# Performance work log

Measured on AMD Instinct MI355X. Metric: run time of the kernel, lower is better.

## Reference

```python
import jax, jax.numpy as jnp
import numpy as np

B, T, C = 4, 2048, 1024
N_HEAD = 16
HEAD_DIM = C // N_HEAD


def setup_inputs() -> dict:
    key = jax.random.key(0)
    k1, k2, k3 = jax.random.split(key, 3)
    scale = 1.0 / np.sqrt(C)
    return {
        "x": jax.random.normal(k1, (B, T, C), dtype=jnp.float32),
        "W_attn": jax.random.normal(k2, (C, 3 * C), dtype=jnp.float32) * scale,
        "b_attn": jnp.zeros((3 * C,), dtype=jnp.float32),
        "W_proj": jax.random.normal(k3, (C, C), dtype=jnp.float32) * scale,
        "b_proj": jnp.zeros((C,), dtype=jnp.float32),
    }


def reference(x, W_attn, b_attn, W_proj, b_proj):
    Bt, Tt, Ct = x.shape
    qkv = x @ W_attn + b_attn                      # [B,T,3C]
    q, k, v = jnp.split(qkv, 3, axis=-1)
    # [B,T,C] -> [B,H,T,D]
    def heads(t):
        return t.reshape(Bt, Tt, N_HEAD, HEAD_DIM).transpose(0, 2, 1, 3)
    q, k, v = heads(q), heads(k), heads(v)
    att = jnp.einsum("bhqd,bhkd->bhqk", q, k) * (1.0 / np.sqrt(HEAD_DIM))
    causal = jnp.tril(jnp.ones((Tt, Tt), dtype=bool))
    att = jnp.where(causal, att, jnp.finfo(att.dtype).min)
    att = jax.nn.softmax(att, axis=-1)
    # dropout = 0.0 (eval mode): identity
    y = jnp.einsum("bhqk,bhkd->bhqd", att, v)      # [B,H,T,D]
    y = y.transpose(0, 2, 1, 3).reshape(Bt, Tt, Ct)
    return y @ W_proj + b_proj
```

## Files before the change

kernel.cpp:

```cpp
#include <hip/hip_runtime.h>
#include <hip/hip_bf16.h>
#include <cstdint>

#define B_SZ 4
#define T_SZ 2048
#define C_SZ 1024
#define H_SZ 16
#define D_SZ 64
#define BT_SZ (B_SZ * T_SZ)
#define C3_SZ (3 * C_SZ)
#define NKC (C_SZ / 32)

typedef __attribute__((ext_vector_type(8))) short bf16x8;
typedef __attribute__((ext_vector_type(4))) float f32x4;
typedef __attribute__((ext_vector_type(4))) unsigned short ushort4v;
typedef __attribute__((ext_vector_type(4))) unsigned int uint4v;

typedef __attribute__((address_space(3))) unsigned int lds_u32;
typedef __attribute__((address_space(1))) const unsigned int glb_u32;

__device__ __forceinline__ unsigned short f2bf(float f) {
  unsigned u = __builtin_bit_cast(unsigned, f);
  u += 0x7fffu + ((u >> 16) & 1u);
  return (unsigned short)(u >> 16);
}

__device__ __forceinline__ unsigned packbf2(float lo, float hi) {
  return __builtin_amdgcn_perm(__builtin_bit_cast(unsigned, hi),
                               __builtin_bit_cast(unsigned, lo), 0x07060302u);
}

__device__ __forceinline__ void gll16(const unsigned short* g,
                                      unsigned short* l) {
  __builtin_amdgcn_global_load_lds((glb_u32*)g, (lds_u32*)l, 16, 0, 0);
}


__device__ __forceinline__ void pack_x_task(const float* __restrict__ x,
                                            unsigned short* __restrict__ Af,
                                            int task, int lane) {
  const int quad = lane >> 4, n = lane & 15;
  const int tb = task >> 5, kc = task & 31;
  const float* src = x + (size_t)(tb * 16 + n) * C_SZ + kc * 32 + quad * 8;
  float4 a = *(const float4*)src;
  float4 b = *(const float4*)(src + 4);
  ushort4v o0, o1;
  o0[0] = f2bf(a.x); o0[1] = f2bf(a.y); o0[2] = f2bf(a.z); o0[3] = f2bf(a.w);
  o1[0] = f2bf(b.x); o1[1] = f2bf(b.y); o1[2] = f2bf(b.z); o1[3] = f2bf(b.w);
  unsigned short* dst = Af + ((size_t)((tb * NKC + kc) * 4 + quad) * 16 + n) * 8;
  *(ushort4v*)dst = o0;
  *(ushort4v*)(dst + 4) = o1;
}

__device__ __forceinline__ void pack_w_task(const float* __restrict__ W,
                                            unsigned short* __restrict__ Wb,
                                            int N, int task, int lane) {
  const int quad = lane >> 4, n = lane & 15;
  const int nt = task >> 5, kc = task & 31;
  const int col = nt * 16 + n;
  const int k0 = kc * 32 + quad * 8;
  ushort4v o0, o1;
#pragma unroll
  for (int i = 0; i < 4; ++i) o0[i] = f2bf(W[(size_t)(k0 + i) * N + col]);
#pragma unroll
  for (int i = 0; i < 4; ++i) o1[i] = f2bf(W[(size_t)(k0 + 4 + i) * N + col]);
  unsigned short* dst = Wb + ((size_t)((nt * NKC + kc) * 4 + quad) * 16 + n) * 8;
  *(ushort4v*)dst = o0;
  *(ushort4v*)(dst + 4) = o1;
}

__global__ __launch_bounds__(256) void pack_all(
    const float* __restrict__ x, const float* __restrict__ Wa,
    const float* __restrict__ Wp, unsigned short* __restrict__ Af,
    unsigned short* __restrict__ Wab, unsigned short* __restrict__ Wpb) {
  const int bx = blockIdx.x;
  const int sub = threadIdx.x >> 6;
  const int lane = threadIdx.x & 63;
  if (bx < 4096) {
    pack_x_task(x, Af, bx * 4 + sub, lane);
  } else if (bx < 4096 + 1536) {
    pack_w_task(Wa, Wab, C3_SZ, (bx - 4096) * 4 + sub, lane);
  } else {
    pack_w_task(Wp, Wpb, C_SZ, (bx - 5632) * 4 + sub, lane);
  }
}

__device__ __forceinline__ void gemm128_mainloop(
    const unsigned short* __restrict__ A, const unsigned short* __restrict__ B,
    int tbB, int ntB, unsigned short* smem, f32x4 acc[4][4]) {
  const int tid = threadIdx.x;
  const int w = tid >> 6, lane = tid & 63;
  const int quad = lane >> 4, n = lane & 15;
  const int wr = w >> 1, wc = w & 1;
  unsigned short* smemA = smem;
  unsigned short* smemB = smem + 8192;

  for (int kc0 = 0; kc0 < NKC; kc0 += 2) {
#pragma unroll
    for (int i2 = 0; i2 < 2; ++i2) {
      const int i = 2 * w + i2;
      const unsigned short* gA =
          A + ((size_t)(tbB + i) * NKC + kc0) * 512 + lane * 8;
      const unsigned short* gB =
          B + ((size_t)(ntB + i) * NKC + kc0) * 512 + lane * 8;
      gll16(gA, smemA + i * 1024);
      gll16(gA + 512, smemA + i * 1024 + 512);
      gll16(gB, smemB + i * 1024);
      gll16(gB + 512, smemB + i * 1024 + 512);
    }
    __syncthreads();
#pragma unroll
    for (int kcl = 0; kcl < 2; ++kcl) {
      bf16x8 af[4], bfr[4];
#pragma unroll
      for (int m = 0; m < 4; ++m)
        af[m] = *(const bf16x8*)(smemA + (wr * 4 + m) * 1024 +
                                 (kcl * 4 + quad) * 128 + n * 8);
#pragma unroll
      for (int nn = 0; nn < 4; ++nn)
        bfr[nn] = *(const bf16x8*)(smemB + (wc * 4 + nn) * 1024 +
                                   (kcl * 4 + quad) * 128 + n * 8);
#pragma unroll
      for (int m = 0; m < 4; ++m)
#pragma unroll
        for (int nn = 0; nn < 4; ++nn)
          acc[m][nn] = __builtin_amdgcn_mfma_f32_16x16x32_bf16(
              af[m], bfr[nn], acc[m][nn], 0, 0, 0);
    }
    __syncthreads();
  }
}

__global__ __launch_bounds__(256) void qkv_mfma(
    const unsigned short* __restrict__ Af, const unsigned short* __restrict__ Wab,
    const float* __restrict__ bias, unsigned short* __restrict__ Qf,
    unsigned short* __restrict__ Kf, unsigned short* __restrict__ Vf) {
  __shared__ unsigned short smem[16384];
  const int tid = threadIdx.x;
  const int w = tid >> 6, lane = tid & 63;
  const int quad = lane >> 4, n = lane & 15;
  const int wr = w >> 1, wc = w & 1;
  const int bx = blockIdx.x, by = blockIdx.y;
  f32x4 acc[4][4];
#pragma unroll
  for (int m = 0; m < 4; ++m)
#pragma unroll
    for (int nn = 0; nn < 4; ++nn) acc[m][nn] = (f32x4){0.f, 0.f, 0.f, 0.f};

  gemm128_mainloop(Af, Wab, by * 8, bx * 8, smem, acc);

  const int cb = bx * 128 + wc * 64;
  const int which = cb >> 10;
  const int h = (cb & 1023) >> 6;
  const int gr0 = by * 128 + wr * 64;
  const int b = gr0 >> 11;
  const int t0 = gr0 & 2047;
  const size_t bhoff = (size_t)(b * H_SZ + h) * (T_SZ * D_SZ);
  float bfl[4];
#pragma unroll
  for (int nn = 0; nn < 4; ++nn) bfl[nn] = bias[cb + nn * 16 + n];

  if (which < 2) {
    unsigned short* dst = ((which == 0) ? Qf : Kf) + bhoff;
    const float scl = (which == 0) ? 0.18033688f : 1.0f;
#pragma unroll
    for (int m = 0; m < 4; ++m) {
      const int tb = (t0 + m * 16) >> 4;
#pragma unroll
      for (int nn = 0; nn < 4; ++nn) {
        const int dc = nn >> 1;
        const int qd = (nn & 1) * 2 + (n >> 3);
        const int jq = n & 7;
#pragma unroll
        for (int r = 0; r < 4; ++r) {
          const int nq = quad * 4 + r;
          dst[((size_t)((tb * 2 + dc) * 4 + qd)) * 128 + nq * 8 + jq] =
              f2bf((acc[m][nn][r] + bfl[nn]) * scl);
        }
      }
    }
  } else {
    unsigned short* dst = Vf + bhoff;
    const int gb0 = t0 >> 5;
#pragma unroll
    for (int m = 0; m < 4; ++m) {
      const int gb = gb0 + (m >> 1);
#pragma unroll
      for (int nn = 0; nn < 4; ++nn) {
#pragma unroll
        for (int r = 0; r < 4; ++r) {
          dst[((size_t)((gb * 4 + nn) * 4 + quad)) * 128 + n * 8 + (m & 1) * 4 + r] =
              f2bf(acc[m][nn][r] + bfl[nn]);
        }
      }
    }
  }
}

__global__ __launch_bounds__(256) void proj_mfma(
    const unsigned short* __restrict__ Yf, const unsigned short* __restrict__ Wpb,
    const float* __restrict__ bias, float* __restrict__ out) {
  __shared__ unsigned short smem[16384];
  const int tid = threadIdx.x;
  const int w = tid >> 6, lane = tid & 63;
  const int quad = lane >> 4, n = lane & 15;
  const int wr = w >> 1, wc = w & 1;
  const int bx = blockIdx.x, by = blockIdx.y;
  f32x4 acc[4][4];
#pragma unroll
  for (int m = 0; m < 4; ++m)
#pragma unroll
    for (int nn = 0; nn < 4; ++nn) acc[m][nn] = (f32x4){0.f, 0.f, 0.f, 0.f};

  gemm128_mainloop(Yf, Wpb, by * 8, bx * 8, smem, acc);

  const int cb = bx * 128 + wc * 64;
  const int gr0 = by * 128 + wr * 64;
  float bfl[4];
#pragma unroll
  for (int nn = 0; nn < 4; ++nn) bfl[nn] = bias[cb + nn * 16 + n];
#pragma unroll
  for (int m = 0; m < 4; ++m)
#pragma unroll
    for (int nn = 0; nn < 4; ++nn)
#pragma unroll
      for (int r = 0; r < 4; ++r)
        out[(size_t)(gr0 + m * 16 + quad * 4 + r) * C_SZ + cb + nn * 16 + n] =
            acc[m][nn][r] + bfl[nn];
}

__global__ __launch_bounds__(64) void attn_mfma(
    const unsigned short* __restrict__ Qf,
    const unsigned short* __restrict__ Kf,
    const unsigned short* __restrict__ Vf, unsigned short* __restrict__ Yf) {
  const int lane = threadIdx.x;
  const int quad = lane >> 4;
  const int n = lane & 15;
  const int bx = blockIdx.x;
  const int qt = 31 - (bx >> 6);
  const int bh = bx & 63;
  const int b = bh >> 4, h = bh & 15;
  const int wq0 = qt * 64;
  const size_t bhoff = (size_t)bh * (T_SZ * D_SZ);
  const bf16x8* Qp = (const bf16x8*)(Qf + bhoff);
  const bf16x8* Kp = (const bf16x8*)(Kf + bhoff);
  const bf16x8* Vp = (const bf16x8*)(Vf + bhoff);

  bf16x8 qfr[4][2];
#pragma unroll
  for (int m = 0; m < 4; ++m) {
    const int tb = (wq0 >> 4) + m;
#pragma unroll
    for (int dc = 0; dc < 2; ++dc)
      qfr[m][dc] = Qp[((tb * 2 + dc) * 4 + quad) * 16 + n];
  }

  bf16x8 kfr[4][2], vfr[2][4];
  f32x4 O[4][4];
  f32x4 ls[4];
#pragma unroll
  for (int m = 0; m < 4; ++m) {
    ls[m] = (f32x4){0.f, 0.f, 0.f, 0.f};
#pragma unroll
    for (int dv = 0; dv < 4; ++dv) O[m][dv] = (f32x4){0.f, 0.f, 0.f, 0.f};
  }

#pragma unroll
  for (int s = 0; s < 4; ++s) {
    kfr[s][0] = Kp[((s * 2 + 0) * 4 + quad) * 16 + n];
    kfr[s][1] = Kp[((s * 2 + 1) * 4 + quad) * 16 + n];
  }

  for (int kt = 0; kt < qt; ++kt) {
#pragma unroll
    for (int g = 0; g < 2; ++g) {
      const int gb = kt * 2 + g;
#pragma unroll
      for (int dv = 0; dv < 4; ++dv)
        vfr[g][dv] = Vp[((gb * 4 + dv) * 4 + quad) * 16 + n];
    }
#pragma unroll
    for (int m = 0; m < 4; ++m) {
      f32x4 st[4];
#pragma unroll
      for (int s = 0; s < 4; ++s) {
        f32x4 z = {0.f, 0.f, 0.f, 0.f};
        z = __builtin_amdgcn_mfma_f32_16x16x32_bf16(kfr[s][0], qfr[m][0], z, 0, 0, 0);
        z = __builtin_amdgcn_mfma_f32_16x16x32_bf16(kfr[s][1], qfr[m][1], z, 0, 0, 0);
        st[s] = z;
      }
      if (m == 3) {
        const int tb0 = (kt + 1) * 4;
#pragma unroll
        for (int s = 0; s < 4; ++s) {
          kfr[s][0] = Kp[(((tb0 + s) * 2 + 0) * 4 + quad) * 16 + n];
          kfr[s][1] = Kp[(((tb0 + s) * 2 + 1) * 4 + quad) * 16 + n];
        }
      }
      uint4v pw[2];
#pragma unroll
      for (int s = 0; s < 4; ++s) {
        float pr[4];
#pragma unroll
        for (int r = 0; r < 4; ++r) {
          pr[r] = __builtin_amdgcn_exp2f(st[s][r]);
          ls[m][r] += pr[r];
        }
        pw[s >> 1][(s & 1) * 2 + 0] = packbf2(pr[0], pr[1]);
        pw[s >> 1][(s & 1) * 2 + 1] = packbf2(pr[2], pr[3]);
      }
#pragma unroll
      for (int g = 0; g < 2; ++g) {
        const bf16x8 pg = __builtin_bit_cast(bf16x8, pw[g]);
#pragma unroll
        for (int dv = 0; dv < 4; ++dv)
          O[m][dv] = __builtin_amdgcn_mfma_f32_16x16x32_bf16(
              pg, vfr[g][dv], O[m][dv], 0, 0, 0);
      }
    }
  }

  {
#pragma unroll
    for (int g = 0; g < 2; ++g) {
      const int gb = qt * 2 + g;
#pragma unroll
      for (int dv = 0; dv < 4; ++dv)
        vfr[g][dv] = Vp[((gb * 4 + dv) * 4 + quad) * 16 + n];
    }
#pragma unroll
    for (int m = 0; m < 4; ++m) {
      f32x4 st[4];
#pragma unroll
      for (int s = 0; s < 4; ++s) {
        f32x4 z = {0.f, 0.f, 0.f, 0.f};
        if (s <= m) {
          z = __builtin_amdgcn_mfma_f32_16x16x32_bf16(kfr[s][0], qfr[m][0], z, 0, 0, 0);
          z = __builtin_amdgcn_mfma_f32_16x16x32_bf16(kfr[s][1], qfr[m][1], z, 0, 0, 0);
        }
        st[s] = z;
      }
      uint4v pw[2] = {(uint4v){0, 0, 0, 0}, (uint4v){0, 0, 0, 0}};
#pragma unroll
      for (int s = 0; s < 4; ++s) {
        if (s <= m) {
          float pr[4];
#pragma unroll
          for (int r = 0; r < 4; ++r) {
            float v = st[s][r];
            if (s == m && quad * 4 + r > n) v = -1e30f;
            pr[r] = __builtin_amdgcn_exp2f(v);
            ls[m][r] += pr[r];
          }
          pw[s >> 1][(s & 1) * 2 + 0] = packbf2(pr[0], pr[1]);
          pw[s >> 1][(s & 1) * 2 + 1] = packbf2(pr[2], pr[3]);
        }
      }
#pragma unroll
      for (int g = 0; g < 2; ++g) {
        if (g * 2 <= m) {
          const bf16x8 pg = __builtin_bit_cast(bf16x8, pw[g]);
#pragma unroll
          for (int dv = 0; dv < 4; ++dv)
            O[m][dv] = __builtin_amdgcn_mfma_f32_16x16x32_bf16(
                pg, vfr[g][dv], O[m][dv], 0, 0, 0);
        }
      }
    }
  }

#pragma unroll
  for (int m = 0; m < 4; ++m) {
    float lt = ls[m][0] + ls[m][1] + ls[m][2] + ls[m][3];
    lt += __shfl_xor(lt, 16);
    lt += __shfl_xor(lt, 32);
    const float inv = 1.0f / lt;
    float iv[4];
#pragma unroll
    for (int r = 0; r < 4; ++r) iv[r] = __shfl(inv, quad * 4 + r);
    const int tb = (b * T_SZ + wq0 + m * 16) >> 4;
#pragma unroll
    for (int dv = 0; dv < 4; ++dv) {
      const int kc = h * 2 + (dv >> 1);
      const int qa = (dv & 1) * 2 + (n >> 3);
      const int ja = n & 7;
#pragma unroll
      for (int r = 0; r < 4; ++r) {
        const int na = quad * 4 + r;
        Yf[((size_t)((tb * NKC + kc) * 4 + qa)) * 128 + na * 8 + ja] =
            f2bf(O[m][dv][r] * iv[r]);
      }
    }
  }
}

extern "C" void kernel_launch(void* const* d_in, const int* in_sizes, int n_in,
                              void* d_out, int out_size, void* d_ws,
                              size_t ws_size, hipStream_t stream) {
  const float* x = (const float*)d_in[0];
  const float* W_attn = (const float*)d_in[1];
  const float* b_attn = (const float*)d_in[2];
  const float* W_proj = (const float*)d_in[3];
  const float* b_proj = (const float*)d_in[4];
  float* out = (float*)d_out;

  const size_t perbf = (size_t)B_SZ * H_SZ * T_SZ * D_SZ;
  unsigned short* Af = (unsigned short*)d_ws;
  unsigned short* Wab = Af + (size_t)BT_SZ * C_SZ;
  unsigned short* Wpb = Wab + (size_t)C_SZ * C3_SZ;
  unsigned short* Qf = Wpb + (size_t)C_SZ * C_SZ;
  unsigned short* Kf = Qf + perbf;
  unsigned short* Vf = Kf + perbf;
  unsigned short* Yf = Vf + perbf;

  pack_all<<<6144, 256, 0, stream>>>(x, W_attn, W_proj, Af, Wab, Wpb);
  qkv_mfma<<<dim3(C3_SZ / 128, BT_SZ / 128), 256, 0, stream>>>(
      Af, Wab, b_attn, Qf, Kf, Vf);
  attn_mfma<<<dim3(32 * B_SZ * H_SZ), 64, 0, stream>>>(Qf, Kf, Vf, Yf);
  proj_mfma<<<dim3(C_SZ / 128, BT_SZ / 128), 256, 0, stream>>>(Yf, Wpb, b_proj,
                                                               out);
}
```

Before: 223.9 us.

## Remap GEMM blocks per XCD for L2 reuse and prefetch V tiles in attention

```diff
diff --git a/kernel.cpp b/kernel.cpp
--- a/kernel.cpp
+++ b/kernel.cpp
@@ -140,7 +140,10 @@
   const int w = tid >> 6, lane = tid & 63;
   const int quad = lane >> 4, n = lane & 15;
   const int wr = w >> 1, wc = w & 1;
-  const int bx = blockIdx.x, by = blockIdx.y;
+  const int f = blockIdx.x;
+  const int xcd = f & 7, i = f >> 3;
+  const int by = xcd * 8 + (i / 24);
+  const int bx = i % 24;
   f32x4 acc[4][4];
 #pragma unroll
   for (int m = 0; m < 4; ++m)
@@ -205,7 +208,10 @@
   const int w = tid >> 6, lane = tid & 63;
   const int quad = lane >> 4, n = lane & 15;
   const int wr = w >> 1, wc = w & 1;
-  const int bx = blockIdx.x, by = blockIdx.y;
+  const int f = blockIdx.x;
+  const int xcd = f & 7, i = f >> 3;
+  const int by = xcd * 8 + (i / 8);
+  const int bx = i % 8;
   f32x4 acc[4][4];
 #pragma unroll
   for (int m = 0; m < 4; ++m)
@@ -229,7 +235,7 @@
             acc[m][nn][r] + bfl[nn];
 }
 
-__global__ __launch_bounds__(64) void attn_mfma(
+__global__ __launch_bounds__(64, 4) void attn_mfma(
     const unsigned short* __restrict__ Qf,
     const unsigned short* __restrict__ Kf,
     const unsigned short* __restrict__ Vf, unsigned short* __restrict__ Yf) {
@@ -270,15 +276,13 @@
     kfr[s][0] = Kp[((s * 2 + 0) * 4 + quad) * 16 + n];
     kfr[s][1] = Kp[((s * 2 + 1) * 4 + quad) * 16 + n];
   }
+#pragma unroll
+  for (int g = 0; g < 2; ++g)
+#pragma unroll
+    for (int dv = 0; dv < 4; ++dv)
+      vfr[g][dv] = Vp[((g * 4 + dv) * 4 + quad) * 16 + n];
 
   for (int kt = 0; kt < qt; ++kt) {
-#pragma unroll
-    for (int g = 0; g < 2; ++g) {
-      const int gb = kt * 2 + g;
-#pragma unroll
-      for (int dv = 0; dv < 4; ++dv)
-        vfr[g][dv] = Vp[((gb * 4 + dv) * 4 + quad) * 16 + n];
-    }
 #pragma unroll
     for (int m = 0; m < 4; ++m) {
       f32x4 st[4];
@@ -317,17 +321,18 @@
           O[m][dv] = __builtin_amdgcn_mfma_f32_16x16x32_bf16(
               pg, vfr[g][dv], O[m][dv], 0, 0, 0);
       }
+      if (m == 3) {
+        const int gb0 = (kt + 1) * 2;
+#pragma unroll
+        for (int g = 0; g < 2; ++g)
+#pragma unroll
+          for (int dv = 0; dv < 4; ++dv)
+            vfr[g][dv] = Vp[(((gb0 + g) * 4 + dv) * 4 + quad) * 16 + n];
+      }
     }
   }
 
   {
-#pragma unroll
-    for (int g = 0; g < 2; ++g) {
-      const int gb = qt * 2 + g;
-#pragma unroll
-      for (int dv = 0; dv < 4; ++dv)
-        vfr[g][dv] = Vp[((gb * 4 + dv) * 4 + quad) * 16 + n];
-    }
 #pragma unroll
     for (int m = 0; m < 4; ++m) {
       f32x4 st[4];
@@ -414,9 +419,7 @@
   unsigned short* Yf = Vf + perbf;
 
   pack_all<<<6144, 256, 0, stream>>>(x, W_attn, W_proj, Af, Wab, Wpb);
-  qkv_mfma<<<dim3(C3_SZ / 128, BT_SZ / 128), 256, 0, stream>>>(
-      Af, Wab, b_attn, Qf, Kf, Vf);
+  qkv_mfma<<<1536, 256, 0, stream>>>(Af, Wab, b_attn, Qf, Kf, Vf);
   attn_mfma<<<dim3(32 * B_SZ * H_SZ), 64, 0, stream>>>(Qf, Kf, Vf, Yf);
-  proj_mfma<<<dim3(C_SZ / 128, BT_SZ / 128), 256, 0, stream>>>(Yf, Wpb, b_proj,
-                                                               out);
-}
+  proj_mfma<<<512, 256, 0, stream>>>(Yf, Wpb, b_proj, out);
+}
```

Result: slower. 577.7 us (+158.0%).

## Split attention KV loop across two waves and combine partials in LDS

Applied to the files above, without the earlier changes.

```diff
diff --git a/kernel.cpp b/kernel.cpp
--- a/kernel.cpp
+++ b/kernel.cpp
@@ -229,11 +229,14 @@
             acc[m][nn][r] + bfl[nn];
 }
 
-__global__ __launch_bounds__(64) void attn_mfma(
+__global__ __launch_bounds__(128) void attn_mfma(
     const unsigned short* __restrict__ Qf,
     const unsigned short* __restrict__ Kf,
     const unsigned short* __restrict__ Vf, unsigned short* __restrict__ Yf) {
-  const int lane = threadIdx.x;
+  __shared__ float comb[64 * 84];
+  const int tid = threadIdx.x;
+  const int w = tid >> 6;
+  const int lane = tid & 63;
   const int quad = lane >> 4;
   const int n = lane & 15;
   const int bx = blockIdx.x;
@@ -246,6 +249,10 @@
   const bf16x8* Kp = (const bf16x8*)(Kf + bhoff);
   const bf16x8* Vp = (const bf16x8*)(Vf + bhoff);
 
+  const int h0 = (qt + 1) >> 1;
+  const int kt_begin = (w == 0) ? 0 : h0;
+  const int kt_end = (w == 0) ? h0 : qt;
+
   bf16x8 qfr[4][2];
 #pragma unroll
   for (int m = 0; m < 4; ++m) {
@@ -267,18 +274,17 @@
 
 #pragma unroll
   for (int s = 0; s < 4; ++s) {
-    kfr[s][0] = Kp[((s * 2 + 0) * 4 + quad) * 16 + n];
-    kfr[s][1] = Kp[((s * 2 + 1) * 4 + quad) * 16 + n];
-  }
-
-  for (int kt = 0; kt < qt; ++kt) {
-#pragma unroll
-    for (int g = 0; g < 2; ++g) {
-      const int gb = kt * 2 + g;
-#pragma unroll
-      for (int dv = 0; dv < 4; ++dv)
-        vfr[g][dv] = Vp[((gb * 4 + dv) * 4 + quad) * 16 + n];
-    }
+    const int tb = kt_begin * 4 + s;
+    kfr[s][0] = Kp[((tb * 2 + 0) * 4 + quad) * 16 + n];
+    kfr[s][1] = Kp[((tb * 2 + 1) * 4 + quad) * 16 + n];
+  }
+#pragma unroll
+  for (int g = 0; g < 2; ++g)
+#pragma unroll
+    for (int dv = 0; dv < 4; ++dv)
+      vfr[g][dv] = Vp[(((kt_begin * 2 + g) * 4 + dv) * 4 + quad) * 16 + n];
+
+  for (int kt = kt_begin; kt < kt_end; ++kt) {
 #pragma unroll
     for (int m = 0; m < 4; ++m) {
       f32x4 st[4];
@@ -317,17 +323,18 @@
           O[m][dv] = __builtin_amdgcn_mfma_f32_16x16x32_bf16(
               pg, vfr[g][dv], O[m][dv], 0, 0, 0);
       }
-    }
-  }
-
-  {
-#pragma unroll
-    for (int g = 0; g < 2; ++g) {
-      const int gb = qt * 2 + g;
-#pragma unroll
-      for (int dv = 0; dv < 4; ++dv)
-        vfr[g][dv] = Vp[((gb * 4 + dv) * 4 + quad) * 16 + n];
-    }
+      if (m == 3) {
+        const int gb0 = (kt + 1) * 2;
+#pragma unroll
+        for (int g = 0; g < 2; ++g)
+#pragma unroll
+          for (int dv = 0; dv < 4; ++dv)
+            vfr[g][dv] = Vp[(((gb0 + g) * 4 + dv) * 4 + quad) * 16 + n];
+      }
+    }
+  }
+
+  if (w == 1) {
 #pragma unroll
     for (int m = 0; m < 4; ++m) {
       f32x4 st[4];
@@ -367,28 +374,53 @@
         }
       }
     }
-  }
-
-#pragma unroll
-  for (int m = 0; m < 4; ++m) {
-    float lt = ls[m][0] + ls[m][1] + ls[m][2] + ls[m][3];
-    lt += __shfl_xor(lt, 16);
-    lt += __shfl_xor(lt, 32);
-    const float inv = 1.0f / lt;
-    float iv[4];
-#pragma unroll
-    for (int r = 0; r < 4; ++r) iv[r] = __shfl(inv, quad * 4 + r);
-    const int tb = (b * T_SZ + wq0 + m * 16) >> 4;
-#pragma unroll
-    for (int dv = 0; dv < 4; ++dv) {
-      const int kc = h * 2 + (dv >> 1);
-      const int qa = (dv & 1) * 2 + (n >> 3);
-      const int ja = n & 7;
-#pragma unroll
-      for (int r = 0; r < 4; ++r) {
-        const int na = quad * 4 + r;
-        Yf[((size_t)((tb * NKC + kc) * 4 + qa)) * 128 + na * 8 + ja] =
-            f2bf(O[m][dv][r] * iv[r]);
+    float* p = comb + lane * 84;
+#pragma unroll
+    for (int m = 0; m < 4; ++m) {
+#pragma unroll
+      for (int dv = 0; dv < 4; ++dv)
+        *(f32x4*)(p + (m * 4 + dv) * 4) = O[m][dv];
+      *(f32x4*)(p + 64 + m * 4) = ls[m];
+    }
+  }
+
+  __syncthreads();
+
+  if (w == 0) {
+    const float* p = comb + lane * 84;
+#pragma unroll
+    for (int m = 0; m < 4; ++m) {
+#pragma unroll
+      for (int dv = 0; dv < 4; ++dv) {
+        f32x4 t = *(const f32x4*)(p + (m * 4 + dv) * 4);
+#pragma unroll
+        for (int r = 0; r < 4; ++r) O[m][dv][r] += t[r];
+      }
+      f32x4 t = *(const f32x4*)(p + 64 + m * 4);
+#pragma unroll
+      for (int r = 0; r < 4; ++r) ls[m][r] += t[r];
+    }
+#pragma unroll
+    for (int m = 0; m < 4; ++m) {
+      float lt = ls[m][0] + ls[m][1] + ls[m][2] + ls[m][3];
+      lt += __shfl_xor(lt, 16);
+      lt += __shfl_xor(lt, 32);
+      const float inv = 1.0f / lt;
+      float iv[4];
+#pragma unroll
+      for (int r = 0; r < 4; ++r) iv[r] = __shfl(inv, quad * 4 + r);
+      const int tb = (b * T_SZ + wq0 + m * 16) >> 4;
+#pragma unroll
+      for (int dv = 0; dv < 4; ++dv) {
+        const int kc = h * 2 + (dv >> 1);
+        const int qa = (dv & 1) * 2 + (n >> 3);
+        const int ja = n & 7;
+#pragma unroll
+        for (int r = 0; r < 4; ++r) {
+          const int na = quad * 4 + r;
+          Yf[((size_t)((tb * NKC + kc) * 4 + qa)) * 128 + na * 8 + ja] =
+              f2bf(O[m][dv][r] * iv[r]);
+        }
       }
     }
   }
@@ -416,7 +448,7 @@
   pack_all<<<6144, 256, 0, stream>>>(x, W_attn, W_proj, Af, Wab, Wpb);
   qkv_mfma<<<dim3(C3_SZ / 128, BT_SZ / 128), 256, 0, stream>>>(
       Af, Wab, b_attn, Qf, Kf, Vf);
-  attn_mfma<<<dim3(32 * B_SZ * H_SZ), 64, 0, stream>>>(Qf, Kf, Vf, Yf);
+  attn_mfma<<<dim3(32 * B_SZ * H_SZ), 128, 0, stream>>>(Qf, Kf, Vf, Yf);
   proj_mfma<<<dim3(C_SZ / 128, BT_SZ / 128), 256, 0, stream>>>(Yf, Wpb, b_proj,
                                                                out);
 }
```

New measurement: 234.3 us. 4.7% more time.
